# Optimization experiments

Hardware: AMD Instinct MI355X
Metric: run time of the kernel (lower is better)

The kernel has to match this reference:

```python
import jax, jax.numpy as jnp
import numpy as np

B, S, D, H, DFF = 2, 2048, 512, 8, 2048
DH = D // H
EPS = 1e-5


def setup_inputs() -> dict:
    key = jax.random.key(0)
    ks = jax.random.split(key, 12)
    g = lambda k, shape, s=0.02: jax.random.normal(k, shape, dtype=jnp.float32) * s
    x = jax.random.normal(ks[0], (B, S, D), dtype=jnp.float32)
    # additive causal mask: 0 on/below diag, -inf above
    neg = jnp.finfo(jnp.float32).min
    attn_mask = jnp.where(jnp.tril(jnp.ones((S, S), dtype=bool)), 0.0, neg).astype(jnp.float32)
    return {
        "x": x,
        "attn_mask": attn_mask,
        "Wq": g(ks[1], (D, D)), "bq": jnp.zeros((D,), jnp.float32),
        "Wk": g(ks[2], (D, D)), "bk": jnp.zeros((D,), jnp.float32),
        "Wv": g(ks[3], (D, D)), "bv": jnp.zeros((D,), jnp.float32),
        "Wo": g(ks[4], (D, D)), "bo": jnp.zeros((D,), jnp.float32),
        "head_alphas": jnp.ones((H,), jnp.float32),
        "ln1_g": jnp.ones((D,), jnp.float32), "ln1_b": jnp.zeros((D,), jnp.float32),
        "W1": g(ks[5], (DFF, D)), "b1": jnp.zeros((DFF,), jnp.float32),
        "W2": g(ks[6], (D, DFF)), "b2": jnp.zeros((D,), jnp.float32),
        "ln2_g": jnp.ones((D,), jnp.float32), "ln2_b": jnp.zeros((D,), jnp.float32),
    }


def _layer_norm(h, g, b):
    mu = jnp.mean(h, axis=-1, keepdims=True)
    var = jnp.mean((h - mu) ** 2, axis=-1, keepdims=True)
    return (h - mu) * jax.lax.rsqrt(var + EPS) * g + b


def reference(x, attn_mask, Wq, bq, Wk, bk, Wv, bv, Wo, bo, head_alphas,
              ln1_g, ln1_b, W1, b1, W2, b2, ln2_g, ln2_b):
    scale = jnp.sqrt(jnp.asarray(DH, dtype=x.dtype))
    # projections (torch Linear: x @ W.T + b)
    q = (x @ Wq.T + bq).reshape(B, S, H, DH).transpose(0, 2, 1, 3)  # bhsd
    k = (x @ Wk.T + bk).reshape(B, S, H, DH).transpose(0, 2, 1, 3)
    v = (x @ Wv.T + bv).reshape(B, S, H, DH).transpose(0, 2, 1, 3)
    attn = jnp.einsum('bhqd,bhkd->bhqk', q, k) / scale
    attn = attn + attn_mask  # broadcast [S,S] over batch/heads
    attn = jax.nn.softmax(attn, axis=-1)
    ctx = jnp.einsum('bhqk,bhkd->bhqd', attn, v)
    ctx = ctx * head_alphas[None, :, None, None]
    ctx = ctx.transpose(0, 2, 1, 3).reshape(B, S, D)
    attn_out = ctx @ Wo.T + bo
    # residual + LN
    h = _layer_norm(x + attn_out, ln1_g, ln1_b)
    # FFN (linear -> ReLU -> linear), residual + LN
    ff = jax.nn.relu(h @ W1.T + b1) @ W2.T + b2
    out = _layer_norm(h + ff, ln2_g, ln2_b)
    return out
```

## Files before the change

kernel.cpp:

```cpp
#include <hip/hip_runtime.h>
#include <hip/hip_bf16.h>
#include <math.h>

#define BB 2
#define SS 2048
#define DD 512
#define HH 8
#define DH 64
#define DFF 2048
#define MM (BB*SS)
#define EPS 1e-5f

typedef __attribute__((ext_vector_type(8))) short bf16x8;
typedef __attribute__((ext_vector_type(4))) float f32x4;

#define GL2LDS(g, l)                                                        \
    __builtin_amdgcn_global_load_lds(                                       \
        (const __attribute__((address_space(1))) void*)(unsigned long long)(g), \
        (__attribute__((address_space(3))) void*)(unsigned int)(unsigned long long)(l), \
        16, 0, 0)

struct Cvt7 {
    const float* s[7];
    unsigned short* d[7];
    unsigned off[8];
};

__global__ __launch_bounds__(256) void cvt_k(Cvt7 a)
{
    unsigned i = blockIdx.x * 256 + threadIdx.x;
    int seg = 0;
    #pragma unroll
    for (int t = 1; t < 7; ++t) seg += (i >= a.off[t]);
    unsigned li = i - a.off[seg];
    float4 v = ((const float4*)a.s[seg])[li];
    union { __hip_bfloat16 h[4]; uint2 u; } t;
    t.h[0] = __float2bfloat16(v.x);
    t.h[1] = __float2bfloat16(v.y);
    t.h[2] = __float2bfloat16(v.z);
    t.h[3] = __float2bfloat16(v.w);
    ((uint2*)a.d[seg])[li] = t.u;
}

template<int TM, int TN>
static __device__ __forceinline__ void gemm_core(
    __hip_bfloat16* As, __hip_bfloat16* Bs,
    const __hip_bfloat16* __restrict__ A, const __hip_bfloat16* __restrict__ Bw,
    const float* __restrict__ bias, const float* __restrict__ resid,
    void* __restrict__ Cout, int N_, int K_, int mode, float oscale)
{
    const int tid   = threadIdx.x;
    const int w     = tid >> 6;
    const int lane  = tid & 63;
    const int quad  = lane >> 4;
    const int col16 = lane & 15;
    const int m0 = blockIdx.y * TM;
    const int n0 = blockIdx.x * TN;
    constexpr int MI = TM / 32;
    constexpr int NJ = TN / 32;
    const int wm = (w >> 1) * (TM / 2);
    const int wn = (w & 1) * (TN / 2);

    const int srow = lane >> 3;
    const int scol = (lane & 7) * 8;
    constexpr int CH_A  = TM / 8;
    constexpr int CH_T  = (TM + TN) / 8;
    constexpr int TPW   = CH_T / 4;

    f32x4 acc[MI][NJ] = {};

    for (int k0 = 0; k0 < K_; k0 += 64) {
        __syncthreads();
        #pragma unroll
        for (int t = 0; t < TPW; ++t) {
            const int c = w * TPW + t;
            if (c < CH_A) {
                GL2LDS(A  + (size_t)(m0 + c*8 + srow) * K_ + k0 + scol,
                       (char*)As + c * 1024);
            } else {
                const int cb = c - CH_A;
                GL2LDS(Bw + (size_t)(n0 + cb*8 + srow) * K_ + k0 + scol,
                       (char*)Bs + cb * 1024);
            }
        }
        __syncthreads();

        #pragma unroll
        for (int kk = 0; kk < 64; kk += 32) {
            bf16x8 af[MI], bf[NJ];
            #pragma unroll
            for (int i = 0; i < MI; ++i)
                af[i] = *(const bf16x8*)(As + (wm + i*16 + col16) * 64 + kk + quad*8);
            #pragma unroll
            for (int j = 0; j < NJ; ++j)
                bf[j] = *(const bf16x8*)(Bs + (wn + j*16 + col16) * 64 + kk + quad*8);
            #pragma unroll
            for (int i = 0; i < MI; ++i)
                #pragma unroll
                for (int j = 0; j < NJ; ++j)
                    acc[i][j] = __builtin_amdgcn_mfma_f32_16x16x32_bf16(
                        af[i], bf[j], acc[i][j], 0, 0, 0);
        }
    }

    #pragma unroll
    for (int i = 0; i < MI; ++i) {
        #pragma unroll
        for (int r = 0; r < 4; ++r) {
            const int m = m0 + wm + i*16 + quad*4 + r;
            #pragma unroll
            for (int j = 0; j < NJ; ++j) {
                const int n = n0 + wn + j*16 + col16;
                float vv = acc[i][j][r] + bias[n];
                if (mode == 0) {
                    size_t idx = (size_t)m * N_ + n;
                    float* Cf = (float*)Cout;
                    if (resid) vv += resid[idx];
                    Cf[idx] = vv;
                } else if (mode == 3) {
                    ((__hip_bfloat16*)Cout)[(size_t)m * N_ + n] =
                        __float2bfloat16(fmaxf(vv, 0.f));
                } else {
                    const int b = m >> 11, s = m & (SS - 1);
                    const int hh = n >> 6, d = n & (DH - 1);
                    if (mode == 1)
                        ((__hip_bfloat16*)Cout)[(((size_t)(b*HH + hh))*SS + s)*DH + d] =
                            __float2bfloat16(vv * oscale);
                    else
                        ((__hip_bfloat16*)Cout)[(((size_t)(b*HH + hh))*DH + d)*SS + s] =
                            __float2bfloat16(vv);
                }
            }
        }
    }
}

__global__ __launch_bounds__(256) void gemm128_k(
    const __hip_bfloat16* __restrict__ A, const __hip_bfloat16* __restrict__ Bw,
    const float* __restrict__ bias, const float* __restrict__ resid,
    void* __restrict__ Cout, int N_, int K_, int mode, float oscale)
{
    __shared__ __hip_bfloat16 As[128*64];
    __shared__ __hip_bfloat16 Bs[128*64];
    gemm_core<128,128>(As, Bs, A, Bw, bias, resid, Cout, N_, K_, mode, oscale);
}

__global__ __launch_bounds__(256) void gemm12864_k(
    const __hip_bfloat16* __restrict__ A, const __hip_bfloat16* __restrict__ Bw,
    const float* __restrict__ bias, const float* __restrict__ resid,
    void* __restrict__ Cout, int N_, int K_, int mode, float oscale)
{
    __shared__ __hip_bfloat16 As[128*64];
    __shared__ __hip_bfloat16 Bs[64*64];
    gemm_core<128,64>(As, Bs, A, Bw, bias, resid, Cout, N_, K_, mode, oscale);
}

__global__ __launch_bounds__(256) void qkv_fused_k(
    const __hip_bfloat16* __restrict__ A, const __hip_bfloat16* __restrict__ Wqkv,
    const float* __restrict__ bq, const float* __restrict__ bk,
    const float* __restrict__ bv,
    __hip_bfloat16* __restrict__ qb, __hip_bfloat16* __restrict__ kb,
    __hip_bfloat16* __restrict__ vtb)
{
    __shared__ __hip_bfloat16 As[128*64];
    __shared__ __hip_bfloat16 Bs[64*64];
    const int tid   = threadIdx.x;
    const int w     = tid >> 6;
    const int lane  = tid & 63;
    const int quad  = lane >> 4;
    const int col16 = lane & 15;
    const int m0 = blockIdx.y * 128;
    const int n0 = blockIdx.x * 64;
    const int wm = (w >> 1) * 64;
    const int wn = (w & 1) * 32;
    const int srow = lane >> 3;
    const int scol = (lane & 7) * 8;

    f32x4 acc[4][2] = {};

    for (int k0 = 0; k0 < DD; k0 += 64) {
        __syncthreads();
        #pragma unroll
        for (int t = 0; t < 6; ++t) {
            const int c = w * 6 + t;
            if (c < 16) {
                GL2LDS(A    + (size_t)(m0 + c*8 + srow) * DD + k0 + scol,
                       (char*)As + c * 1024);
            } else {
                const int cb = c - 16;
                GL2LDS(Wqkv + (size_t)(n0 + cb*8 + srow) * DD + k0 + scol,
                       (char*)Bs + cb * 1024);
            }
        }
        __syncthreads();

        #pragma unroll
        for (int kk = 0; kk < 64; kk += 32) {
            bf16x8 af[4], bf[2];
            #pragma unroll
            for (int i = 0; i < 4; ++i)
                af[i] = *(const bf16x8*)(As + (wm + i*16 + col16) * 64 + kk + quad*8);
            #pragma unroll
            for (int j = 0; j < 2; ++j)
                bf[j] = *(const bf16x8*)(Bs + (wn + j*16 + col16) * 64 + kk + quad*8);
            #pragma unroll
            for (int i = 0; i < 4; ++i)
                #pragma unroll
                for (int j = 0; j < 2; ++j)
                    acc[i][j] = __builtin_amdgcn_mfma_f32_16x16x32_bf16(
                        af[i], bf[j], acc[i][j], 0, 0, 0);
        }
    }

    const int z = n0 >> 9;
    const float* bias = (z == 0) ? bq : (z == 1) ? bk : bv;
    __hip_bfloat16* dst = (z == 0) ? qb : (z == 1) ? kb : vtb;
    const float sc = (z == 0) ? 0.125f : 1.0f;
    #pragma unroll
    for (int i = 0; i < 4; ++i) {
        #pragma unroll
        for (int r = 0; r < 4; ++r) {
            const int m = m0 + wm + i*16 + quad*4 + r;
            const int b = m >> 11, s = m & (SS - 1);
            #pragma unroll
            for (int j = 0; j < 2; ++j) {
                const int n  = n0 + wn + j*16 + col16;
                const int nn = n & 511;
                const int hh = nn >> 6, d = nn & (DH - 1);
                float vv = (acc[i][j][r] + bias[nn]) * sc;
                if (z < 2)
                    dst[(((size_t)(b*HH + hh))*SS + s)*DH + d] = __float2bfloat16(vv);
                else
                    dst[(((size_t)(b*HH + hh))*DH + d)*SS + s] = __float2bfloat16(vv);
            }
        }
    }
}

__global__ __launch_bounds__(512) void attn_mfma_k(
    const __hip_bfloat16* __restrict__ Q,
    const __hip_bfloat16* __restrict__ K,
    const __hip_bfloat16* __restrict__ VT,
    const float* __restrict__ halpha,
    __hip_bfloat16* __restrict__ ctx)
{
    const int w    = threadIdx.x >> 6;
    const int lane = threadIdx.x & 63;
    const int quad = lane >> 4;
    const int col  = lane & 15;
    const int bh   = blockIdx.x;
    const int b    = bh >> 3, h = bh & 7;
    const int qt   = gridDim.y - 1 - blockIdx.y;
    const int q0   = qt * 64;
    const int nchunk = qt + 1;

    const __hip_bfloat16* Qbh = Q  + (size_t)bh * SS * DH;
    const __hip_bfloat16* Kbh = K  + (size_t)bh * SS * DH;
    const __hip_bfloat16* Vbh = VT + (size_t)bh * DH * SS;

    __shared__ float smem[16896];
    __hip_bfloat16* bb     = (__hip_bfloat16*)smem;
    __hip_bfloat16* p_base = bb + (size_t)w * 4096;
    float* lbuf = smem + 16384;

    bf16x8 qf[4][2];
    #pragma unroll
    for (int mi = 0; mi < 4; ++mi) {
        const __hip_bfloat16* qp = Qbh + (size_t)(q0 + mi*16 + col) * DH + quad * 8;
        qf[mi][0] = *(const bf16x8*)(qp);
        qf[mi][1] = *(const bf16x8*)(qp + 32);
    }

    f32x4 acc_o[4][4] = {};
    float lp[4][4] = {};

    for (int c = w; c < nchunk; c += 8) {
        const int k0 = c * 64;
        const bool diag = (c == qt);

        #pragma unroll
        for (int ks = 0; ks < 4; ++ks) {
            const __hip_bfloat16* kp = Kbh + (size_t)(k0 + ks*16 + col) * DH + quad * 8;
            bf16x8 kb0 = *(const bf16x8*)(kp);
            bf16x8 kb1 = *(const bf16x8*)(kp + 32);
            const int keyl = ks*16 + col;
            const int kh = keyl >> 5;
            const int lr = ((keyl >> 3) & 3) * 16;
            const int j  = keyl & 7;
            const int kg = k0 + keyl;
            #pragma unroll
            for (int mi = 0; mi < 4; ++mi) {
                f32x4 s = {};
                s = __builtin_amdgcn_mfma_f32_16x16x32_bf16(qf[mi][0], kb0, s, 0, 0, 0);
                s = __builtin_amdgcn_mfma_f32_16x16x32_bf16(qf[mi][1], kb1, s, 0, 0, 0);
                #pragma unroll
                for (int r = 0; r < 4; ++r) {
                    float p;
                    if (diag) {
                        int qg = q0 + mi*16 + quad*4 + r;
                        p = (kg > qg) ? 0.f : __expf(s[r]);
                    } else {
                        p = __expf(s[r]);
                    }
                    lp[mi][r] += p;
                    p_base[mi*1024 + kh*512 + (lr + quad*4 + r)*8 + j] =
                        __float2bfloat16(p);
                }
            }
        }

        bf16x8 pa[4][2];
        #pragma unroll
        for (int mi = 0; mi < 4; ++mi) {
            pa[mi][0] = *(const bf16x8*)(p_base + mi*1024 + lane*8);
            pa[mi][1] = *(const bf16x8*)(p_base + mi*1024 + 512 + lane*8);
        }
        #pragma unroll
        for (int d = 0; d < 4; ++d) {
            const __hip_bfloat16* vp = Vbh + (size_t)(d*16 + col) * SS + k0 + quad * 8;
            bf16x8 vb0 = *(const bf16x8*)(vp);
            bf16x8 vb1 = *(const bf16x8*)(vp + 32);
            #pragma unroll
            for (int mi = 0; mi < 4; ++mi) {
                acc_o[mi][d] = __builtin_amdgcn_mfma_f32_16x16x32_bf16(pa[mi][0], vb0, acc_o[mi][d], 0, 0, 0);
                acc_o[mi][d] = __builtin_amdgcn_mfma_f32_16x16x32_bf16(pa[mi][1], vb1, acc_o[mi][d], 0, 0, 0);
            }
        }
    }

    #pragma unroll
    for (int mi = 0; mi < 4; ++mi)
        #pragma unroll
        for (int r = 0; r < 4; ++r) {
            float s_ = lp[mi][r];
            #pragma unroll
            for (int o = 1; o < 16; o <<= 1) s_ += __shfl_xor(s_, o);
            lp[mi][r] = s_;
        }

    __syncthreads();
    __hip_bfloat16* obuf = bb + (size_t)w * 4096;
    #pragma unroll
    for (int mi = 0; mi < 4; ++mi)
        #pragma unroll
        for (int d = 0; d < 4; ++d)
            #pragma unroll
            for (int r = 0; r < 4; ++r)
                obuf[(mi*16 + quad*4 + r)*64 + d*16 + col] =
                    __float2bfloat16(acc_o[mi][d][r]);
    if (col == 0) {
        #pragma unroll
        for (int mi = 0; mi < 4; ++mi)
            #pragma unroll
            for (int r = 0; r < 4; ++r)
                lbuf[w*64 + mi*16 + quad*4 + r] = lp[mi][r];
    }
    __syncthreads();

    const float ha = halpha[h];
    #pragma unroll
    for (int rr = 0; rr < 8; ++rr) {
        const int row = w*8 + rr;
        float L = 0.f, val = 0.f;
        #pragma unroll
        for (int p = 0; p < 8; ++p) {
            L   += lbuf[p*64 + row];
            val += __bfloat162float(bb[p*4096 + row*64 + lane]);
        }
        ctx[((size_t)(b*SS + q0 + row))*DD + h*64 + lane] =
            __float2bfloat16(val * ha / L);
    }
}

__global__ __launch_bounds__(256) void ln_k(
    const float* __restrict__ in, const float* __restrict__ g,
    const float* __restrict__ bta, float* __restrict__ out,
    __hip_bfloat16* __restrict__ outb)
{
    const int row = blockIdx.x;
    const float* p = in + (size_t)row * DD;
    const int t = threadIdx.x;
    float v0 = p[t], v1 = p[t + 256];
    __shared__ float red[256];
    red[t] = v0 + v1;
    __syncthreads();
    for (int o = 128; o > 0; o >>= 1) { if (t < o) red[t] += red[t + o]; __syncthreads(); }
    float mu = red[0] * (1.f / DD);
    __syncthreads();
    float d0 = v0 - mu, d1 = v1 - mu;
    red[t] = d0*d0 + d1*d1;
    __syncthreads();
    for (int o = 128; o > 0; o >>= 1) { if (t < o) red[t] += red[t + o]; __syncthreads(); }
    float rstd = rsqrtf(red[0] * (1.f / DD) + EPS);
    float o0 = d0 * rstd * g[t]       + bta[t];
    float o1 = d1 * rstd * g[t + 256] + bta[t + 256];
    out[(size_t)row * DD + t]       = o0;
    out[(size_t)row * DD + t + 256] = o1;
    if (outb) {
        outb[(size_t)row * DD + t]       = __float2bfloat16(o0);
        outb[(size_t)row * DD + t + 256] = __float2bfloat16(o1);
    }
}

extern "C" void kernel_launch(void* const* d_in, const int* in_sizes, int n_in,
                              void* d_out, int out_size, void* d_ws, size_t ws_size,
                              hipStream_t stream)
{
    const float* x    = (const float*)d_in[0];
    const float* Wq   = (const float*)d_in[2];
    const float* bq   = (const float*)d_in[3];
    const float* Wk   = (const float*)d_in[4];
    const float* bk   = (const float*)d_in[5];
    const float* Wv   = (const float*)d_in[6];
    const float* bv   = (const float*)d_in[7];
    const float* Wo   = (const float*)d_in[8];
    const float* bo   = (const float*)d_in[9];
    const float* hal  = (const float*)d_in[10];
    const float* ln1g = (const float*)d_in[11];
    const float* ln1b = (const float*)d_in[12];
    const float* W1   = (const float*)d_in[13];
    const float* b1   = (const float*)d_in[14];
    const float* W2   = (const float*)d_in[15];
    const float* b2   = (const float*)d_in[16];
    const float* ln2g = (const float*)d_in[17];
    const float* ln2b = (const float*)d_in[18];
    float* out = (float*)d_out;

    char* ws = (char*)d_ws;
    const size_t MB = 1ull << 20;
    __hip_bfloat16* Wqb = (__hip_bfloat16*)(ws);
    __hip_bfloat16* Wkb = (__hip_bfloat16*)(ws + MB/2);
    __hip_bfloat16* Wvb = (__hip_bfloat16*)(ws + MB);
    __hip_bfloat16* Wob = (__hip_bfloat16*)(ws + MB + MB/2);
    __hip_bfloat16* W1b = (__hip_bfloat16*)(ws + 2*MB);
    __hip_bfloat16* W2b = (__hip_bfloat16*)(ws + 4*MB);
    __hip_bfloat16* xb  = (__hip_bfloat16*)(ws + 6*MB);
    __hip_bfloat16* qb  = (__hip_bfloat16*)(ws + 10*MB);
    __hip_bfloat16* kb  = (__hip_bfloat16*)(ws + 14*MB);
    __hip_bfloat16* vtb = (__hip_bfloat16*)(ws + 18*MB);
    __hip_bfloat16* ctxb= (__hip_bfloat16*)(ws + 22*MB);
    float* h1  = (float*)(ws + 26*MB);
    float* h   = (float*)(ws + 34*MB);
    __hip_bfloat16* hb  = (__hip_bfloat16*)(ws + 42*MB);
    __hip_bfloat16* ff1b= (__hip_bfloat16*)(ws + 10*MB);
    float* f2  = (float*)(ws + 26*MB);

    dim3 blk(256);

    Cvt7 ca;
    ca.s[0] = x;  ca.d[0] = (unsigned short*)xb;
    ca.s[1] = Wq; ca.d[1] = (unsigned short*)Wqb;
    ca.s[2] = Wk; ca.d[2] = (unsigned short*)Wkb;
    ca.s[3] = Wv; ca.d[3] = (unsigned short*)Wvb;
    ca.s[4] = Wo; ca.d[4] = (unsigned short*)Wob;
    ca.s[5] = W1; ca.d[5] = (unsigned short*)W1b;
    ca.s[6] = W2; ca.d[6] = (unsigned short*)W2b;
    unsigned offs[8] = {0, 524288, 589824, 655360, 720896, 786432, 1048576, 1310720};
    for (int i = 0; i < 8; ++i) ca.off[i] = offs[i];
    cvt_k<<<dim3(5120), blk, 0, stream>>>(ca);

    qkv_fused_k<<<dim3((3*DD)/64, MM/128), blk, 0, stream>>>(
        xb, Wqb, bq, bk, bv, qb, kb, vtb);

    attn_mfma_k<<<dim3(BB*HH, SS/64), dim3(512), 0, stream>>>(
        qb, kb, vtb, hal, ctxb);

    gemm12864_k<<<dim3(DD/64, MM/128), blk, 0, stream>>>(
        ctxb, Wob, bo, x, h1, DD, DD, 0, 1.0f);
    ln_k<<<dim3(MM), blk, 0, stream>>>(h1, ln1g, ln1b, h, hb);

    gemm128_k<<<dim3(DFF/128, MM/128), blk, 0, stream>>>(
        hb, W1b, b1, nullptr, ff1b, DFF, DD, 3, 1.0f);
    gemm12864_k<<<dim3(DD/64, MM/128), blk, 0, stream>>>(
        ff1b, W2b, b2, h, f2, DD, DFF, 0, 1.0f);
    ln_k<<<dim3(MM), blk, 0, stream>>>(f2, ln2g, ln2b, out, nullptr);
}
```

Baseline: 268.0 us.

## Shrink GEMM tiles to 64x64 and split-K output projections with LN-fused reduction

All GEMMs now use 64x64 tiles, giving more workgroups to fill the CUs. The Wo and W2 projections use a 2-way split-K that writes fp32 partial sums. A new LayerNorm kernel then adds the two partials, bias and residual before normalising. This targets under-occupancy of the small-M GEMMs, at the cost of extra fp32 partial traffic and less data reuse per tile.

```diff
diff --git a/kernel.cpp b/kernel.cpp
--- a/kernel.cpp
+++ b/kernel.cpp
@@ -42,74 +42,66 @@
     ((uint2*)a.d[seg])[li] = t.u;
 }
 
-template<int TM, int TN>
-static __device__ __forceinline__ void gemm_core(
-    __hip_bfloat16* As, __hip_bfloat16* Bs,
+__global__ __launch_bounds__(256) void gemm64_k(
     const __hip_bfloat16* __restrict__ A, const __hip_bfloat16* __restrict__ Bw,
     const float* __restrict__ bias, const float* __restrict__ resid,
     void* __restrict__ Cout, int N_, int K_, int mode, float oscale)
 {
+    __shared__ __hip_bfloat16 As[64*64];
+    __shared__ __hip_bfloat16 Bs[64*64];
     const int tid   = threadIdx.x;
     const int w     = tid >> 6;
     const int lane  = tid & 63;
     const int quad  = lane >> 4;
     const int col16 = lane & 15;
-    const int m0 = blockIdx.y * TM;
-    const int n0 = blockIdx.x * TN;
-    constexpr int MI = TM / 32;
-    constexpr int NJ = TN / 32;
-    const int wm = (w >> 1) * (TM / 2);
-    const int wn = (w & 1) * (TN / 2);
-
+    const int m0 = blockIdx.y * 64;
+    const int n0 = blockIdx.x * 64;
+    const int wm = (w >> 1) * 32;
+    const int wn = (w & 1) * 32;
     const int srow = lane >> 3;
     const int scol = (lane & 7) * 8;
-    constexpr int CH_A  = TM / 8;
-    constexpr int CH_T  = (TM + TN) / 8;
-    constexpr int TPW   = CH_T / 4;
-
-    f32x4 acc[MI][NJ] = {};
+
+    f32x4 acc[2][2] = {};
 
     for (int k0 = 0; k0 < K_; k0 += 64) {
         __syncthreads();
         #pragma unroll
-        for (int t = 0; t < TPW; ++t) {
-            const int c = w * TPW + t;
-            if (c < CH_A) {
+        for (int t = 0; t < 4; ++t) {
+            const int c = w * 4 + t;
+            if (c < 8)
                 GL2LDS(A  + (size_t)(m0 + c*8 + srow) * K_ + k0 + scol,
                        (char*)As + c * 1024);
-            } else {
-                const int cb = c - CH_A;
-                GL2LDS(Bw + (size_t)(n0 + cb*8 + srow) * K_ + k0 + scol,
-                       (char*)Bs + cb * 1024);
-            }
+            else
+                GL2LDS(Bw + (size_t)(n0 + (c-8)*8 + srow) * K_ + k0 + scol,
+                       (char*)Bs + (c-8) * 1024);
         }
         __syncthreads();
 
         #pragma unroll
         for (int kk = 0; kk < 64; kk += 32) {
-            bf16x8 af[MI], bf[NJ];
-            #pragma unroll
-            for (int i = 0; i < MI; ++i)
+            bf16x8 af[2], bf[2];
+            #pragma unroll
+            for (int i = 0; i < 2; ++i)
                 af[i] = *(const bf16x8*)(As + (wm + i*16 + col16) * 64 + kk + quad*8);
             #pragma unroll
-            for (int j = 0; j < NJ; ++j)
+            for (int j = 0; j < 2; ++j)
                 bf[j] = *(const bf16x8*)(Bs + (wn + j*16 + col16) * 64 + kk + quad*8);
             #pragma unroll
-            for (int i = 0; i < MI; ++i)
+            for (int i = 0; i < 2; ++i)
                 #pragma unroll
-                for (int j = 0; j < NJ; ++j)
+                for (int j = 0; j < 2; ++j)
                     acc[i][j] = __builtin_amdgcn_mfma_f32_16x16x32_bf16(
                         af[i], bf[j], acc[i][j], 0, 0, 0);
         }
     }
 
     #pragma unroll
-    for (int i = 0; i < MI; ++i) {
+    for (int i = 0; i < 2; ++i) {
         #pragma unroll
         for (int r = 0; r < 4; ++r) {
             const int m = m0 + wm + i*16 + quad*4 + r;
             #pragma unroll
-            for (int j = 0; j < NJ; ++j) {
+            for (int j = 0; j < 2; ++j) {
                 const int n = n0 + wn + j*16 + col16;
                 float vv = acc[i][j][r] + bias[n];
                 if (mode == 0) {
@@ -117,94 +109,61 @@
                     float* Cf = (float*)Cout;
                     if (resid) vv += resid[idx];
                     Cf[idx] = vv;
-                } else if (mode == 3) {
+                } else {
                     ((__hip_bfloat16*)Cout)[(size_t)m * N_ + n] =
-                        __float2bfloat16(fmaxf(vv, 0.f));
-                } else {
-                    const int b = m >> 11, s = m & (SS - 1);
-                    const int hh = n >> 6, d = n & (DH - 1);
-                    if (mode == 1)
-                        ((__hip_bfloat16*)Cout)[(((size_t)(b*HH + hh))*SS + s)*DH + d] =
-                            __float2bfloat16(vv * oscale);
-                    else
-                        ((__hip_bfloat16*)Cout)[(((size_t)(b*HH + hh))*DH + d)*SS + s] =
-                            __float2bfloat16(vv);
+                        __float2bfloat16(fmaxf(vv, 0.f) * oscale);
                 }
             }
         }
     }
 }
 
-__global__ __launch_bounds__(256) void gemm128_k(
+__global__ __launch_bounds__(256) void gemm64sk_k(
     const __hip_bfloat16* __restrict__ A, const __hip_bfloat16* __restrict__ Bw,
-    const float* __restrict__ bias, const float* __restrict__ resid,
-    void* __restrict__ Cout, int N_, int K_, int mode, float oscale)
-{
-    __shared__ __hip_bfloat16 As[128*64];
-    __shared__ __hip_bfloat16 Bs[128*64];
-    gemm_core<128,128>(As, Bs, A, Bw, bias, resid, Cout, N_, K_, mode, oscale);
-}
-
-__global__ __launch_bounds__(256) void gemm12864_k(
-    const __hip_bfloat16* __restrict__ A, const __hip_bfloat16* __restrict__ Bw,
-    const float* __restrict__ bias, const float* __restrict__ resid,
-    void* __restrict__ Cout, int N_, int K_, int mode, float oscale)
-{
-    __shared__ __hip_bfloat16 As[128*64];
-    __shared__ __hip_bfloat16 Bs[64*64];
-    gemm_core<128,64>(As, Bs, A, Bw, bias, resid, Cout, N_, K_, mode, oscale);
-}
-
-__global__ __launch_bounds__(256) void qkv_fused_k(
-    const __hip_bfloat16* __restrict__ A, const __hip_bfloat16* __restrict__ Wqkv,
-    const float* __restrict__ bq, const float* __restrict__ bk,
-    const float* __restrict__ bv,
-    __hip_bfloat16* __restrict__ qb, __hip_bfloat16* __restrict__ kb,
-    __hip_bfloat16* __restrict__ vtb)
-{
-    __shared__ __hip_bfloat16 As[128*64];
+    float* __restrict__ part, int N_, int Ktot, int Kseg)
+{
+    __shared__ __hip_bfloat16 As[64*64];
     __shared__ __hip_bfloat16 Bs[64*64];
     const int tid   = threadIdx.x;
     const int w     = tid >> 6;
     const int lane  = tid & 63;
     const int quad  = lane >> 4;
     const int col16 = lane & 15;
-    const int m0 = blockIdx.y * 128;
+    const int m0 = blockIdx.y * 64;
     const int n0 = blockIdx.x * 64;
-    const int wm = (w >> 1) * 64;
+    const int wm = (w >> 1) * 32;
     const int wn = (w & 1) * 32;
     const int srow = lane >> 3;
     const int scol = (lane & 7) * 8;
-
-    f32x4 acc[4][2] = {};
-
-    for (int k0 = 0; k0 < DD; k0 += 64) {
+    const int kbeg = blockIdx.z * Kseg;
+
+    f32x4 acc[2][2] = {};
+
+    for (int k0 = kbeg; k0 < kbeg + Kseg; k0 += 64) {
         __syncthreads();
         #pragma unroll
-        for (int t = 0; t < 6; ++t) {
-            const int c = w * 6 + t;
-            if (c < 16) {
-                GL2LDS(A    + (size_t)(m0 + c*8 + srow) * DD + k0 + scol,
+        for (int t = 0; t < 4; ++t) {
+            const int c = w * 4 + t;
+            if (c < 8)
+                GL2LDS(A  + (size_t)(m0 + c*8 + srow) * Ktot + k0 + scol,
                        (char*)As + c * 1024);
-            } else {
-                const int cb = c - 16;
-                GL2LDS(Wqkv + (size_t)(n0 + cb*8 + srow) * DD + k0 + scol,
-                       (char*)Bs + cb * 1024);
-            }
+            else
+                GL2LDS(Bw + (size_t)(n0 + (c-8)*8 + srow) * Ktot + k0 + scol,
+                       (char*)Bs + (c-8) * 1024);
         }
         __syncthreads();
 
         #pragma unroll
         for (int kk = 0; kk < 64; kk += 32) {
-            bf16x8 af[4], bf[2];
-            #pragma unroll
-            for (int i = 0; i < 4; ++i)
+            bf16x8 af[2], bf[2];
+            #pragma unroll
+            for (int i = 0; i < 2; ++i)
                 af[i] = *(const bf16x8*)(As + (wm + i*16 + col16) * 64 + kk + quad*8);
             #pragma unroll
             for (int j = 0; j < 2; ++j)
                 bf[j] = *(const bf16x8*)(Bs + (wn + j*16 + col16) * 64 + kk + quad*8);
             #pragma unroll
-            for (int i = 0; i < 4; ++i)
+            for (int i = 0; i < 2; ++i)
                 #pragma unroll
                 for (int j = 0; j < 2; ++j)
                     acc[i][j] = __builtin_amdgcn_mfma_f32_16x16x32_bf16(
@@ -212,12 +171,81 @@
         }
     }
 
+    float* dst = part + (size_t)blockIdx.z * MM * N_;
+    #pragma unroll
+    for (int i = 0; i < 2; ++i)
+        #pragma unroll
+        for (int r = 0; r < 4; ++r) {
+            const int m = m0 + wm + i*16 + quad*4 + r;
+            #pragma unroll
+            for (int j = 0; j < 2; ++j) {
+                const int n = n0 + wn + j*16 + col16;
+                dst[(size_t)m * N_ + n] = acc[i][j][r];
+            }
+        }
+}
+
+__global__ __launch_bounds__(256) void qkv64_k(
+    const __hip_bfloat16* __restrict__ A, const __hip_bfloat16* __restrict__ Wqkv,
+    const float* __restrict__ bq, const float* __restrict__ bk,
+    const float* __restrict__ bv,
+    __hip_bfloat16* __restrict__ qb, __hip_bfloat16* __restrict__ kb,
+    __hip_bfloat16* __restrict__ vtb)
+{
+    __shared__ __hip_bfloat16 As[64*64];
+    __shared__ __hip_bfloat16 Bs[64*64];
+    const int tid   = threadIdx.x;
+    const int w     = tid >> 6;
+    const int lane  = tid & 63;
+    const int quad  = lane >> 4;
+    const int col16 = lane & 15;
+    const int m0 = blockIdx.y * 64;
+    const int n0 = blockIdx.x * 64;
+    const int wm = (w >> 1) * 32;
+    const int wn = (w & 1) * 32;
+    const int srow = lane >> 3;
+    const int scol = (lane & 7) * 8;
+
+    f32x4 acc[2][2] = {};
+
+    for (int k0 = 0; k0 < DD; k0 += 64) {
+        __syncthreads();
+        #pragma unroll
+        for (int t = 0; t < 4; ++t) {
+            const int c = w * 4 + t;
+            if (c < 8)
+                GL2LDS(A    + (size_t)(m0 + c*8 + srow) * DD + k0 + scol,
+                       (char*)As + c * 1024);
+            else
+                GL2LDS(Wqkv + (size_t)(n0 + (c-8)*8 + srow) * DD + k0 + scol,
+                       (char*)Bs + (c-8) * 1024);
+        }
+        __syncthreads();
+
+        #pragma unroll
+        for (int kk = 0; kk < 64; kk += 32) {
+            bf16x8 af[2], bf[2];
+            #pragma unroll
+            for (int i = 0; i < 2; ++i)
+                af[i] = *(const bf16x8*)(As + (wm + i*16 + col16) * 64 + kk + quad*8);
+            #pragma unroll
+            for (int j = 0; j < 2; ++j)
+                bf[j] = *(const bf16x8*)(Bs + (wn + j*16 + col16) * 64 + kk + quad*8);
+            #pragma unroll
+            for (int i = 0; i < 2; ++i)
+                #pragma unroll
+                for (int j = 0; j < 2; ++j)
+                    acc[i][j] = __builtin_amdgcn_mfma_f32_16x16x32_bf16(
+                        af[i], bf[j], acc[i][j], 0, 0, 0);
+        }
+    }
+
     const int z = n0 >> 9;
     const float* bias = (z == 0) ? bq : (z == 1) ? bk : bv;
     __hip_bfloat16* dst = (z == 0) ? qb : (z == 1) ? kb : vtb;
     const float sc = (z == 0) ? 0.125f : 1.0f;
     #pragma unroll
-    for (int i = 0; i < 4; ++i) {
+    for (int i = 0; i < 2; ++i)
         #pragma unroll
         for (int r = 0; r < 4; ++r) {
             const int m = m0 + wm + i*16 + quad*4 + r;
@@ -234,7 +262,6 @@
                     dst[(((size_t)(b*HH + hh))*DH + d)*SS + s] = __float2bfloat16(vv);
             }
         }
-    }
 }
 
 __global__ __launch_bounds__(512) void attn_mfma_k(
@@ -372,15 +399,17 @@
     }
 }
 
-__global__ __launch_bounds__(256) void ln_k(
-    const float* __restrict__ in, const float* __restrict__ g,
-    const float* __restrict__ bta, float* __restrict__ out,
-    __hip_bfloat16* __restrict__ outb)
+__global__ __launch_bounds__(256) void ln_red_k(
+    const float* __restrict__ pa, const float* __restrict__ pb,
+    const float* __restrict__ bias, const float* __restrict__ resid,
+    const float* __restrict__ g, const float* __restrict__ bta,
+    float* __restrict__ out, __hip_bfloat16* __restrict__ outb)
 {
     const int row = blockIdx.x;
-    const float* p = in + (size_t)row * DD;
+    const size_t base = (size_t)row * DD;
     const int t = threadIdx.x;
-    float v0 = p[t], v1 = p[t + 256];
+    float v0 = pa[base + t]       + pb[base + t]       + bias[t]       + resid[base + t];
+    float v1 = pa[base + t + 256] + pb[base + t + 256] + bias[t + 256] + resid[base + t + 256];
     __shared__ float red[256];
     red[t] = v0 + v1;
     __syncthreads();
@@ -394,11 +423,11 @@
     float rstd = rsqrtf(red[0] * (1.f / DD) + EPS);
     float o0 = d0 * rstd * g[t]       + bta[t];
     float o1 = d1 * rstd * g[t + 256] + bta[t + 256];
-    out[(size_t)row * DD + t]       = o0;
-    out[(size_t)row * DD + t + 256] = o1;
+    out[base + t]       = o0;
+    out[base + t + 256] = o1;
     if (outb) {
-        outb[(size_t)row * DD + t]       = __float2bfloat16(o0);
-        outb[(size_t)row * DD + t + 256] = __float2bfloat16(o1);
+        outb[base + t]       = __float2bfloat16(o0);
+        outb[base + t + 256] = __float2bfloat16(o1);
     }
 }
 
@@ -428,30 +457,28 @@
 
     char* ws = (char*)d_ws;
     const size_t MB = 1ull << 20;
-    __hip_bfloat16* Wqb = (__hip_bfloat16*)(ws);
-    __hip_bfloat16* Wkb = (__hip_bfloat16*)(ws + MB/2);
-    __hip_bfloat16* Wvb = (__hip_bfloat16*)(ws + MB);
-    __hip_bfloat16* Wob = (__hip_bfloat16*)(ws + MB + MB/2);
-    __hip_bfloat16* W1b = (__hip_bfloat16*)(ws + 2*MB);
-    __hip_bfloat16* W2b = (__hip_bfloat16*)(ws + 4*MB);
-    __hip_bfloat16* xb  = (__hip_bfloat16*)(ws + 6*MB);
-    __hip_bfloat16* qb  = (__hip_bfloat16*)(ws + 10*MB);
-    __hip_bfloat16* kb  = (__hip_bfloat16*)(ws + 14*MB);
-    __hip_bfloat16* vtb = (__hip_bfloat16*)(ws + 18*MB);
-    __hip_bfloat16* ctxb= (__hip_bfloat16*)(ws + 22*MB);
-    float* h1  = (float*)(ws + 26*MB);
-    float* h   = (float*)(ws + 34*MB);
-    __hip_bfloat16* hb  = (__hip_bfloat16*)(ws + 42*MB);
-    __hip_bfloat16* ff1b= (__hip_bfloat16*)(ws + 10*MB);
-    float* f2  = (float*)(ws + 26*MB);
+    __hip_bfloat16* Wqkv = (__hip_bfloat16*)(ws);
+    __hip_bfloat16* Wob  = (__hip_bfloat16*)(ws + MB + MB/2);
+    __hip_bfloat16* W1b  = (__hip_bfloat16*)(ws + 2*MB);
+    __hip_bfloat16* W2b  = (__hip_bfloat16*)(ws + 4*MB);
+    __hip_bfloat16* xb   = (__hip_bfloat16*)(ws + 6*MB);
+    __hip_bfloat16* qb   = (__hip_bfloat16*)(ws + 10*MB);
+    __hip_bfloat16* kb   = (__hip_bfloat16*)(ws + 14*MB);
+    __hip_bfloat16* vtb  = (__hip_bfloat16*)(ws + 18*MB);
+    __hip_bfloat16* ctxb = (__hip_bfloat16*)(ws + 22*MB);
+    float* part = (float*)(ws + 26*MB);
+    float* h    = (float*)(ws + 42*MB);
+    __hip_bfloat16* hb   = (__hip_bfloat16*)(ws + 22*MB);
+    __hip_bfloat16* ff1b = (__hip_bfloat16*)(ws + 6*MB);
 
     dim3 blk(256);
+    const size_t PSEG = (size_t)MM * DD;
 
     Cvt7 ca;
     ca.s[0] = x;  ca.d[0] = (unsigned short*)xb;
-    ca.s[1] = Wq; ca.d[1] = (unsigned short*)Wqb;
-    ca.s[2] = Wk; ca.d[2] = (unsigned short*)Wkb;
-    ca.s[3] = Wv; ca.d[3] = (unsigned short*)Wvb;
+    ca.s[1] = Wq; ca.d[1] = (unsigned short*)Wqkv;
+    ca.s[2] = Wk; ca.d[2] = (unsigned short*)(Wqkv + 512*512);
+    ca.s[3] = Wv; ca.d[3] = (unsigned short*)(Wqkv + 2*512*512);
     ca.s[4] = Wo; ca.d[4] = (unsigned short*)Wob;
     ca.s[5] = W1; ca.d[5] = (unsigned short*)W1b;
     ca.s[6] = W2; ca.d[6] = (unsigned short*)W2b;
@@ -459,19 +486,22 @@
     for (int i = 0; i < 8; ++i) ca.off[i] = offs[i];
     cvt_k<<<dim3(5120), blk, 0, stream>>>(ca);
 
-    qkv_fused_k<<<dim3((3*DD)/64, MM/128), blk, 0, stream>>>(
-        xb, Wqb, bq, bk, bv, qb, kb, vtb);
+    qkv64_k<<<dim3((3*DD)/64, MM/64), blk, 0, stream>>>(
+        xb, Wqkv, bq, bk, bv, qb, kb, vtb);
 
     attn_mfma_k<<<dim3(BB*HH, SS/64), dim3(512), 0, stream>>>(
         qb, kb, vtb, hal, ctxb);
 
-    gemm12864_k<<<dim3(DD/64, MM/128), blk, 0, stream>>>(
-        ctxb, Wob, bo, x, h1, DD, DD, 0, 1.0f);
-    ln_k<<<dim3(MM), blk, 0, stream>>>(h1, ln1g, ln1b, h, hb);
-
-    gemm128_k<<<dim3(DFF/128, MM/128), blk, 0, stream>>>(
+    gemm64sk_k<<<dim3(DD/64, MM/64, 2), blk, 0, stream>>>(
+        ctxb, Wob, part, DD, DD, 256);
+    ln_red_k<<<dim3(MM), blk, 0, stream>>>(
+        part, part + PSEG, bo, x, ln1g, ln1b, h, hb);
+
+    gemm64_k<<<dim3(DFF/64, MM/64), blk, 0, stream>>>(
         hb, W1b, b1, nullptr, ff1b, DFF, DD, 3, 1.0f);
-    gemm12864_k<<<dim3(DD/64, MM/128), blk, 0, stream>>>(
-        ff1b, W2b, b2, h, f2, DD, DFF, 0, 1.0f);
-    ln_k<<<dim3(MM), blk, 0, stream>>>(f2, ln2g, ln2b, out, nullptr);
-}
+
+    gemm64sk_k<<<dim3(DD/64, MM/64, 2), blk, 0, stream>>>(
+        ff1b, W2b, part, DD, DFF, 1024);
+    ln_red_k<<<dim3(MM), blk, 0, stream>>>(
+        part, part + PSEG, b2, h, ln2g, ln2b, out, nullptr);
+}
```

After: 237.4 us. 11.4% less time.
